# Optimization experiments

Hardware: AMD Instinct MI355X
Metric: run time of the kernel (lower is better)

The kernel has to match this reference:

```python
import jax, jax.numpy as jnp
import numpy as np

N, K, DN, DA, H = 20000, 16, 128, 128, 256
D_IN = DN + DA  # 256


def _lin_init(key, out_dim, in_dim):
    scale = 1.0 / np.sqrt(in_dim)
    return jax.random.uniform(key, (out_dim, in_dim), jnp.float32, -scale, scale)


def setup_inputs() -> dict:
    key = jax.random.key(0)
    ks = jax.random.split(key, 16)
    # adjacency: col 0 = parent index; cols 1..K = neighbor indices, -1 padded.
    parent = jax.random.randint(ks[0], (N, 1), 0, N, dtype=jnp.int32)
    nbr_first = jax.random.randint(ks[1], (N, 1), 0, N, dtype=jnp.int32)  # guarantee >=1 nbr
    nbr_rest = jax.random.randint(ks[2], (N, K - 1), -1, N, dtype=jnp.int32)
    adj = jnp.concatenate([parent, nbr_first, nbr_rest], axis=1)
    names = jax.random.normal(ks[3], (N, DN), jnp.float32)
    attrs = jax.random.normal(ks[4], (N, DA), jnp.float32)
    return {
        "nodeAdjacencySpecTensor": adj,
        "nodeNamesEncoded": names,
        "nodeAttributesEncoded": attrs,
        "W_in": _lin_init(ks[5], H, D_IN),
        "b_in": jnp.zeros((H,), jnp.float32),
        "W_parent": _lin_init(ks[6], H, H),
        "b_parent": jnp.zeros((H,), jnp.float32),
        "W_neighbor": _lin_init(ks[7], H, H),
        "b_neighbor": jnp.zeros((H,), jnp.float32),
        "W_ih": _lin_init(ks[8], 3 * H, H),
        "b_ih": jnp.zeros((3 * H,), jnp.float32),
        "W_hh": _lin_init(ks[9], 3 * H, H),
        "b_hh": jnp.zeros((3 * H,), jnp.float32),
        "depth": 3,
    }


def _gru_cell(x, h, W_ih, b_ih, W_hh, b_hh):
    # torch.nn.GRUCell math; gate order r, z, n.
    gi = x @ W_ih.T + b_ih
    gh = h @ W_hh.T + b_hh
    i_r, i_z, i_n = jnp.split(gi, 3, axis=-1)
    h_r, h_z, h_n = jnp.split(gh, 3, axis=-1)
    r = jax.nn.sigmoid(i_r + h_r)
    z = jax.nn.sigmoid(i_z + h_z)
    n = jnp.tanh(i_n + r * h_n)
    return (1.0 - z) * n + z * h


def reference(nodeAdjacencySpecTensor, nodeNamesEncoded, nodeAttributesEncoded,
              W_in, b_in, W_parent, b_parent, W_neighbor, b_neighbor,
              W_ih, b_ih, W_hh, b_hh, depth):
    adj = nodeAdjacencySpecTensor
    parent_idx = adj[:, 0]                 # [N]
    nbr_idx = adj[:, 1:]                   # [N, K], -1 padded
    mask = (nbr_idx >= 0)                  # [N, K]
    safe_nbr = jnp.clip(nbr_idx, 0, None)
    nbr_count = jnp.maximum(mask.sum(axis=1), 1).astype(jnp.float32)  # [N]

    node_info = jnp.concatenate([nodeNamesEncoded, nodeAttributesEncoded], axis=-1)
    x = node_info @ W_in.T + b_in          # [N, H]

    for _ in range(depth):
        p = x @ W_parent.T + b_parent      # [N, H]
        nbr = x @ W_neighbor.T + b_neighbor  # [N, H]
        # irregular gathers
        parent_feat = p[parent_idx]        # [N, H]
        gathered = nbr[safe_nbr]           # [N, K, H]
        nbr_sum = jnp.sum(gathered * mask[:, :, None], axis=1)  # [N, H]
        summary = parent_feat + nbr_sum / nbr_count[:, None]
        x = _gru_cell(x, summary, W_ih, b_ih, W_hh, b_hh)
    return x
```

## Files before the change

kernel.cpp:

```cpp
#include <hip/hip_runtime.h>
#include <hip/hip_bf16.h>

typedef __bf16 bf16x8 __attribute__((ext_vector_type(8)));
typedef __bf16 bf16x4 __attribute__((ext_vector_type(4)));
typedef float  f32x4  __attribute__((ext_vector_type(4)));

#define NN   20000
#define NADJ 17

__device__ __forceinline__ void xcd_remap(int b, int nwg, int col_shift, int& r, int& c)
{
    int q = nwg >> 3, rem = nwg & 7;
    int x = b & 7, k = b >> 3;
    int start = x * q + (x < rem ? x : rem);
    int idx = start + k;
    r = idx >> col_shift;
    c = idx & ((1 << col_shift) - 1);
}

__global__ void pack_weights_kernel(const float* __restrict__ Win, const float* __restrict__ bin,
                                    const float* __restrict__ Wp,  const float* __restrict__ bp,
                                    const float* __restrict__ Wn,  const float* __restrict__ bn,
                                    const float* __restrict__ Wih, const float* __restrict__ bih,
                                    const float* __restrict__ Whh, const float* __restrict__ bhh,
                                    __bf16* __restrict__ Wb, float* __restrict__ bc)
{
    int idx = blockIdx.x * 256 + threadIdx.x;
    if (idx < 1536) {
        int c = idx; float v;
        if (c < 256)      v = bin[c];
        else if (c < 512) { int j = c - 256; v = bp[j] + bn[j]; }
        else {
            int rel = c - 512;
            int j = (rel >> 6) * 16 + (rel & 15);
            int g = (rel >> 4) & 3;
            if      (g == 0) v = bih[j] + bhh[j];
            else if (g == 1) v = bih[256 + j] + bhh[256 + j];
            else if (g == 2) v = bih[512 + j];
            else             v = bhh[512 + j];
        }
        bc[c] = v;
    }
    if (idx >= 180224) return;
    int e = idx << 2;
    const float* src = nullptr;
    bool zero = false;
    if (e < 65536) {
        int row = e >> 8, k = e & 255;
        src = Win + (size_t)row * 256 + k;
    } else if (e < 196608) {
        int rel = e - 65536;
        int row = rel >> 9, k = rel & 511;
        src = (k < 256) ? (Wp + (size_t)row * 256 + k)
                        : (Wn + (size_t)row * 256 + (k - 256));
    } else {
        int rel = e - 196608;
        int row = rel >> 9, k = rel & 511;
        int j = (row >> 6) * 16 + (row & 15);
        int g = (row >> 4) & 3;
        if (k < 256) {
            if (g == 3) zero = true;
            else {
                int off = (g == 0) ? 0 : (g == 1) ? 256 : 512;
                src = Wih + (size_t)(off + j) * 256 + k;
            }
        } else {
            int k2 = k - 256;
            if (g == 2) zero = true;
            else {
                int off = (g == 0) ? 0 : (g == 1) ? 256 : 512;
                src = Whh + (size_t)(off + j) * 256 + k2;
            }
        }
    }
    float4 v = zero ? make_float4(0.f, 0.f, 0.f, 0.f) : *(const float4*)src;
    bf16x4 o = { (__bf16)v.x, (__bf16)v.y, (__bf16)v.z, (__bf16)v.w };
    *(bf16x4*)(Wb + (size_t)e) = o;
}

__global__ void pack_info_kernel(const float* __restrict__ names, const float* __restrict__ attrs,
                                 __bf16* __restrict__ xb)
{
    int idx = blockIdx.x * 256 + threadIdx.x;
    if (idx >= NN * 64) return;
    int i  = idx >> 6;
    int d4 = (idx & 63) << 2;
    const float* src = (d4 < 128) ? (names + (size_t)i * 128 + d4)
                                  : (attrs + (size_t)i * 128 + (d4 - 128));
    float4 v = *(const float4*)src;
    bf16x4 o = { (__bf16)v.x, (__bf16)v.y, (__bf16)v.z, (__bf16)v.w };
    *(bf16x4*)(xb + (size_t)i * 256 + d4) = o;
}

__global__ void gather_avg_kernel(const int* __restrict__ adj, const __bf16* __restrict__ x,
                                  __bf16* __restrict__ G2)
{
    const int node = blockIdx.x * 4 + (threadIdx.x >> 6);
    const int l = threadIdx.x & 63;
    int av = (l < NADJ) ? adj[(size_t)node * NADJ + l] : -1;
    float s0 = 0.f, s1 = 0.f, s2 = 0.f, s3 = 0.f;
    int cnt = 0;
#pragma unroll
    for (int j = 1; j < NADJ; ++j) {
        int idx = __shfl(av, j, 64);
        if (idx >= 0) {
            ++cnt;
            bf16x4 v = *(const bf16x4*)(x + (size_t)idx * 256 + l * 4);
            s0 += (float)v[0]; s1 += (float)v[1]; s2 += (float)v[2]; s3 += (float)v[3];
        }
    }
    float inv = 1.f / (float)(cnt < 1 ? 1 : cnt);
    bf16x4 o = { (__bf16)(s0 * inv), (__bf16)(s1 * inv), (__bf16)(s2 * inv), (__bf16)(s3 * inv) };
    *(bf16x4*)(G2 + (size_t)node * 256 + l * 4) = o;
}

__global__ __launch_bounds__(256, 4)
void gemm_bias_kernel(const __bf16* __restrict__ A0, const __bf16* __restrict__ A1, int lda,
                      const int* __restrict__ parents, int par_stride,
                      const __bf16* __restrict__ W, int ldw,
                      const float* __restrict__ bias,
                      float* __restrict__ C, __bf16* __restrict__ Cb,
                      int n_rows, int n_cols, int kt_n, int nwg, int col_shift)
{
    __shared__ __align__(16) __bf16 As[128 * 64];
    __shared__ __align__(16) __bf16 Bs[128 * 64];
    __shared__ int par_s[128];
    const int t = threadIdx.x;
    const int w = t >> 6;
    const int l = t & 63;
    int rb, cb_;
    xcd_remap(blockIdx.x, nwg, col_shift, rb, cb_);
    const int brow = rb * 128;
    const int bcol = cb_ * 128;
    const int wr = (w >> 1) * 64, wc = (w & 1) * 64;

    if (parents) {
        if (t < 128) {
            int node = brow + t; if (node > n_rows - 1) node = n_rows - 1;
            par_s[t] = parents[(size_t)node * par_stride];
        }
        __syncthreads();
    }

    f32x4 acc[4][4] = {};

    for (int kt = 0; kt < kt_n; ++kt) {
        const int k0 = kt * 64;
#pragma unroll
        for (int i = 0; i < 4; ++i) {
            int f   = i * 256 + t;
            int row = f >> 3;
            int cs  = ((f & 7) * 16) ^ ((row & 7) << 4);
            int ar  = brow + row; if (ar > n_rows - 1) ar = n_rows - 1;
            const __bf16* abase;
            if (parents && k0 < 256)             abase = A0 + (size_t)par_s[row] * 256 + k0;
            else if (A1 != nullptr && k0 >= 256) abase = A1 + (size_t)ar * 256 + (k0 - 256);
            else                                 abase = A0 + (size_t)ar * lda + k0;
            const __bf16* ga = abase + (cs >> 1);
            const __bf16* gb = W + (size_t)(bcol + row) * ldw + k0 + (cs >> 1);
            char* la = (char*)As + (i * 256 + w * 64) * 16;
            char* lb = (char*)Bs + (i * 256 + w * 64) * 16;
            __builtin_amdgcn_global_load_lds(
                (const __attribute__((address_space(1))) unsigned int*)ga,
                (__attribute__((address_space(3))) unsigned int*)la, 16, 0, 0);
            __builtin_amdgcn_global_load_lds(
                (const __attribute__((address_space(1))) unsigned int*)gb,
                (__attribute__((address_space(3))) unsigned int*)lb, 16, 0, 0);
        }
        asm volatile("s_waitcnt vmcnt(0)" ::: "memory");
        __syncthreads();
#pragma unroll
        for (int ks = 0; ks < 2; ++ks) {
            bf16x8 af[4], bfv[4];
#pragma unroll
            for (int m = 0; m < 4; ++m) {
                int row = wr + m * 16 + (l & 15);
                int cb  = (ks * 64 + ((l >> 4) * 16)) ^ ((row & 7) << 4);
                af[m] = *(const bf16x8*)((const char*)As + row * 128 + cb);
            }
#pragma unroll
            for (int n = 0; n < 4; ++n) {
                int row = wc + n * 16 + (l & 15);
                int cb  = (ks * 64 + ((l >> 4) * 16)) ^ ((row & 7) << 4);
                bfv[n] = *(const bf16x8*)((const char*)Bs + row * 128 + cb);
            }
#pragma unroll
            for (int m = 0; m < 4; ++m)
#pragma unroll
                for (int n = 0; n < 4; ++n)
                    acc[m][n] = __builtin_amdgcn_mfma_f32_16x16x32_bf16(af[m], bfv[n], acc[m][n], 0, 0, 0);
        }
        __syncthreads();
    }
#pragma unroll
    for (int m = 0; m < 4; ++m) {
        int r0 = brow + wr + m * 16 + ((l >> 4) * 4);
#pragma unroll
        for (int n = 0; n < 4; ++n) {
            int c = bcol + wc + n * 16 + (l & 15);
            float bv = bias[c];
#pragma unroll
            for (int i = 0; i < 4; ++i) {
                int r = r0 + i;
                if (r < n_rows) {
                    float v = acc[m][n][i] + bv;
                    if (C)  C[(size_t)r * n_cols + c]  = v;
                    if (Cb) Cb[(size_t)r * n_cols + c] = (__bf16)v;
                }
            }
        }
    }
}

#define GRU_KT_BODY(K0, ABASE, SKIP_N)                                                  \
    {                                                                                   \
        _Pragma("unroll")                                                               \
        for (int i = 0; i < 4; ++i) {                                                   \
            int f   = i * 256 + t;                                                      \
            int row = f >> 3;                                                           \
            int cs  = ((f & 7) * 16) ^ ((row & 7) << 4);                                \
            int ar  = brow + row; if (ar > n_rows - 1) ar = n_rows - 1;                 \
            const __bf16* ga = (ABASE) + (size_t)ar * 256 + (cs >> 1);                  \
            const __bf16* gb = W + (size_t)(bcol + row) * 512 + (K0) + (cs >> 1);       \
            char* la = (char*)As + (i * 256 + w * 64) * 16;                             \
            char* lb = (char*)Bs + (i * 256 + w * 64) * 16;                             \
            __builtin_amdgcn_global_load_lds(                                           \
                (const __attribute__((address_space(1))) unsigned int*)ga,              \
                (__attribute__((address_space(3))) unsigned int*)la, 16, 0, 0);         \
            if (((row >> 4) & 3) != (SKIP_N))                                           \
                __builtin_amdgcn_global_load_lds(                                       \
                    (const __attribute__((address_space(1))) unsigned int*)gb,          \
                    (__attribute__((address_space(3))) unsigned int*)lb, 16, 0, 0);     \
        }                                                                               \
        asm volatile("s_waitcnt vmcnt(0)" ::: "memory");                                \
        __syncthreads();                                                                \
        _Pragma("unroll")                                                               \
        for (int ks = 0; ks < 2; ++ks) {                                                \
            bf16x8 af[4], bfv[4];                                                       \
            _Pragma("unroll")                                                           \
            for (int m = 0; m < 4; ++m) {                                               \
                int row = wr + m * 16 + (l & 15);                                       \
                int cb  = (ks * 64 + ((l >> 4) * 16)) ^ ((row & 7) << 4);               \
                af[m] = *(const bf16x8*)((const char*)As + row * 128 + cb);             \
            }                                                                           \
            _Pragma("unroll")                                                           \
            for (int n = 0; n < 4; ++n) {                                               \
                if (n == (SKIP_N)) continue;                                            \
                int row = wc + n * 16 + (l & 15);                                       \
                int cb  = (ks * 64 + ((l >> 4) * 16)) ^ ((row & 7) << 4);               \
                bfv[n] = *(const bf16x8*)((const char*)Bs + row * 128 + cb);            \
            }                                                                           \
            _Pragma("unroll")                                                           \
            for (int m = 0; m < 4; ++m)                                                 \
                _Pragma("unroll")                                                       \
                for (int n = 0; n < 4; ++n)                                             \
                    if (n != (SKIP_N))                                                  \
                        acc[m][n] = __builtin_amdgcn_mfma_f32_16x16x32_bf16(            \
                            af[m], bfv[n], acc[m][n], 0, 0, 0);                         \
        }                                                                               \
        __syncthreads();                                                                \
    }

__global__ __launch_bounds__(256, 4)
void gru_gemm_kernel(const __bf16* __restrict__ A0, const __bf16* __restrict__ A1,
                     const __bf16* __restrict__ W,
                     const float* __restrict__ bias,
                     const float* __restrict__ SUM,
                     float* __restrict__ X, __bf16* __restrict__ xb_next,
                     int n_rows)
{
    __shared__ __align__(16) __bf16 As[128 * 64];
    __shared__ __align__(16) __bf16 Bs[128 * 64];
    const int t = threadIdx.x;
    const int w = t >> 6;
    const int l = t & 63;
    int rb, cb_;
    xcd_remap(blockIdx.x, 157 * 8, 3, rb, cb_);
    const int brow = rb * 128;
    const int bcol = cb_ * 128;
    const int wr = (w >> 1) * 64, wc = (w & 1) * 64;

    f32x4 acc[4][4] = {};

    for (int kt = 0; kt < 4; ++kt) {
        const int k0 = kt * 64;
        GRU_KT_BODY(k0, A0 + k0, 3)
    }
    for (int kt = 4; kt < 8; ++kt) {
        const int k0 = kt * 64;
        GRU_KT_BODY(k0, A1 + (k0 - 256), 2)
    }

    const int jb = ((bcol + wc) >> 6) * 16 + (l & 15);
    const int c0 = bcol + wc + (l & 15);
    const float b0 = bias[c0], b1 = bias[c0 + 16], b2 = bias[c0 + 32], b3 = bias[c0 + 48];
#pragma unroll
    for (int m = 0; m < 4; ++m) {
        int r0 = brow + wr + m * 16 + ((l >> 4) * 4);
#pragma unroll
        for (int i = 0; i < 4; ++i) {
            int r = r0 + i;
            if (r < n_rows) {
                float gr  = acc[m][0][i] + b0;
                float gz  = acc[m][1][i] + b1;
                float gin = acc[m][2][i] + b2;
                float ghn = acc[m][3][i] + b3;
                float rg = 1.f / (1.f + __expf(-gr));
                float zg = 1.f / (1.f + __expf(-gz));
                float a2 = gin + rg * ghn;
                float tt = __expf(-2.f * fabsf(a2));
                float ng = (1.f - tt) / (1.f + tt);
                ng = (a2 < 0.f) ? -ng : ng;
                float h = SUM[(size_t)r * 256 + jb];
                float out = (1.f - zg) * ng + zg * h;
                if (X)       X[(size_t)r * 256 + jb] = out;
                if (xb_next) xb_next[(size_t)r * 256 + jb] = (__bf16)out;
            }
        }
    }
}

extern "C" void kernel_launch(void* const* d_in, const int* in_sizes, int n_in,
                              void* d_out, int out_size, void* d_ws, size_t ws_size,
                              hipStream_t stream)
{
    const int*   adj   = (const int*)  d_in[0];
    const float* names = (const float*)d_in[1];
    const float* attrs = (const float*)d_in[2];
    const float* Win = (const float*)d_in[3];
    const float* bin = (const float*)d_in[4];
    const float* Wp  = (const float*)d_in[5];
    const float* bp  = (const float*)d_in[6];
    const float* Wn  = (const float*)d_in[7];
    const float* bn  = (const float*)d_in[8];
    const float* Wih = (const float*)d_in[9];
    const float* bih = (const float*)d_in[10];
    const float* Whh = (const float*)d_in[11];
    const float* bhh = (const float*)d_in[12];
    float* X = (float*)d_out;

    char* w = (char*)d_ws;
    __bf16* xinfo = (__bf16*)(w);
    __bf16* xb0   = (__bf16*)(w + 10240000);
    __bf16* xb1   = (__bf16*)(w + 20480000);
    __bf16* sb    = (__bf16*)(w + 30720000);
    __bf16* G2    = (__bf16*)(w + 40960000);
    float*  SUM   = (float*) (w + 51200000);
    __bf16* Wb    = (__bf16*)(w + 71680000);
    float*  bc    = (float*) (w + 73121792);

    pack_weights_kernel<<<704, 256, 0, stream>>>(Win, bin, Wp, bp, Wn, bn, Wih, bih, Whh, bhh, Wb, bc);
    pack_info_kernel<<<5000, 256, 0, stream>>>(names, attrs, xinfo);

    gemm_bias_kernel<<<314, 256, 0, stream>>>(xinfo, nullptr, 256, nullptr, 0,
                                              Wb, 256, bc, nullptr, xb0, NN, 256, 4, 314, 1);

    __bf16* cur = xb0;
    __bf16* nxt = xb1;
    for (int d = 0; d < 3; ++d) {
        gather_avg_kernel<<<5000, 256, 0, stream>>>(adj, cur, G2);
        gemm_bias_kernel<<<314, 256, 0, stream>>>(cur, G2, 256, adj, NADJ,
                                                  Wb + 65536, 512, bc + 256,
                                                  SUM, sb, NN, 256, 8, 314, 1);
        gru_gemm_kernel<<<1256, 256, 0, stream>>>(cur, sb, Wb + 196608, bc + 512,
                                                  SUM, (d == 2) ? X : nullptr,
                                                  (d < 2) ? nxt : nullptr, NN);
        __bf16* tmp = cur; cur = nxt; nxt = tmp;
    }
}
```

Baseline: 265.4 us.

## Fuse neighbor gather-average into summary GEMM and split summary into bf16 hi/lo

Each summary-GEMM block now gathers and averages its 64 rows' neighbor features straight into LDS, then runs the parent/neighbor GEMM with a full 256-column weight tile. This removes the separate gather kernel and the G2 round trip through global memory. The fp32 SUM buffer is replaced by a bf16 hi/lo pair, which cuts write traffic while keeping near-fp32 precision for the GRU hidden term. In exchange, the fused kernel runs only 313 blocks of 512 threads with large LDS use, so occupancy and latency hiding may be limited.

Result: slower. 314.0 us (+18.3%).

```diff
diff --git a/kernel.cpp b/kernel.cpp
--- a/kernel.cpp
+++ b/kernel.cpp
@@ -92,39 +92,15 @@
     *(bf16x4*)(xb + (size_t)i * 256 + d4) = o;
 }
 
-__global__ void gather_avg_kernel(const int* __restrict__ adj, const __bf16* __restrict__ x,
-                                  __bf16* __restrict__ G2)
-{
-    const int node = blockIdx.x * 4 + (threadIdx.x >> 6);
-    const int l = threadIdx.x & 63;
-    int av = (l < NADJ) ? adj[(size_t)node * NADJ + l] : -1;
-    float s0 = 0.f, s1 = 0.f, s2 = 0.f, s3 = 0.f;
-    int cnt = 0;
-#pragma unroll
-    for (int j = 1; j < NADJ; ++j) {
-        int idx = __shfl(av, j, 64);
-        if (idx >= 0) {
-            ++cnt;
-            bf16x4 v = *(const bf16x4*)(x + (size_t)idx * 256 + l * 4);
-            s0 += (float)v[0]; s1 += (float)v[1]; s2 += (float)v[2]; s3 += (float)v[3];
-        }
-    }
-    float inv = 1.f / (float)(cnt < 1 ? 1 : cnt);
-    bf16x4 o = { (__bf16)(s0 * inv), (__bf16)(s1 * inv), (__bf16)(s2 * inv), (__bf16)(s3 * inv) };
-    *(bf16x4*)(G2 + (size_t)node * 256 + l * 4) = o;
-}
-
 __global__ __launch_bounds__(256, 4)
-void gemm_bias_kernel(const __bf16* __restrict__ A0, const __bf16* __restrict__ A1, int lda,
-                      const int* __restrict__ parents, int par_stride,
+void gemm_bias_kernel(const __bf16* __restrict__ A0, int lda,
                       const __bf16* __restrict__ W, int ldw,
                       const float* __restrict__ bias,
-                      float* __restrict__ C, __bf16* __restrict__ Cb,
+                      __bf16* __restrict__ Cb,
                       int n_rows, int n_cols, int kt_n, int nwg, int col_shift)
 {
     __shared__ __align__(16) __bf16 As[128 * 64];
     __shared__ __align__(16) __bf16 Bs[128 * 64];
-    __shared__ int par_s[128];
     const int t = threadIdx.x;
     const int w = t >> 6;
     const int l = t & 63;
@@ -134,14 +110,6 @@
     const int bcol = cb_ * 128;
     const int wr = (w >> 1) * 64, wc = (w & 1) * 64;
 
-    if (parents) {
-        if (t < 128) {
-            int node = brow + t; if (node > n_rows - 1) node = n_rows - 1;
-            par_s[t] = parents[(size_t)node * par_stride];
-        }
-        __syncthreads();
-    }
-
     f32x4 acc[4][4] = {};
 
     for (int kt = 0; kt < kt_n; ++kt) {
@@ -152,11 +120,7 @@
             int row = f >> 3;
             int cs  = ((f & 7) * 16) ^ ((row & 7) << 4);
             int ar  = brow + row; if (ar > n_rows - 1) ar = n_rows - 1;
-            const __bf16* abase;
-            if (parents && k0 < 256)             abase = A0 + (size_t)par_s[row] * 256 + k0;
-            else if (A1 != nullptr && k0 >= 256) abase = A1 + (size_t)ar * 256 + (k0 - 256);
-            else                                 abase = A0 + (size_t)ar * lda + k0;
-            const __bf16* ga = abase + (cs >> 1);
+            const __bf16* ga = A0 + (size_t)ar * lda + k0 + (cs >> 1);
             const __bf16* gb = W + (size_t)(bcol + row) * ldw + k0 + (cs >> 1);
             char* la = (char*)As + (i * 256 + w * 64) * 16;
             char* lb = (char*)Bs + (i * 256 + w * 64) * 16;
@@ -202,10 +166,118 @@
 #pragma unroll
             for (int i = 0; i < 4; ++i) {
                 int r = r0 + i;
+                if (r < n_rows) Cb[(size_t)r * n_cols + c] = (__bf16)(acc[m][n][i] + bv);
+            }
+        }
+    }
+}
+
+__global__ __launch_bounds__(512, 4)
+void summary_fused_kernel(const int* __restrict__ adj, const __bf16* __restrict__ x,
+                          const __bf16* __restrict__ Wps, const float* __restrict__ bias,
+                          __bf16* __restrict__ sbh, __bf16* __restrict__ sbl, int n_rows)
+{
+    __shared__ __align__(16) __bf16 Gs[4 * 64 * 64];
+    __shared__ __align__(16) __bf16 As[64 * 64];
+    __shared__ __align__(16) __bf16 Bs[256 * 64];
+    __shared__ int par_s[64];
+    const int t = threadIdx.x;
+    const int w = t >> 6;
+    const int l = t & 63;
+    const int brow = blockIdx.x * 64;
+
+#pragma unroll
+    for (int q = 0; q < 8; ++q) {
+        int rr = w * 8 + q;
+        int node = brow + rr; if (node > n_rows - 1) node = n_rows - 1;
+        int av = (l < NADJ) ? adj[(size_t)node * NADJ + l] : -1;
+        if (l == 0) par_s[rr] = av;
+        float s0 = 0.f, s1 = 0.f, s2 = 0.f, s3 = 0.f;
+        int cnt = 0;
+#pragma unroll
+        for (int j = 1; j < NADJ; ++j) {
+            int idx = __shfl(av, j, 64);
+            if (idx >= 0) {
+                ++cnt;
+                bf16x4 v = *(const bf16x4*)(x + (size_t)idx * 256 + l * 4);
+                s0 += (float)v[0]; s1 += (float)v[1]; s2 += (float)v[2]; s3 += (float)v[3];
+            }
+        }
+        float inv = 1.f / (float)(cnt < 1 ? 1 : cnt);
+        bf16x4 o = { (__bf16)(s0 * inv), (__bf16)(s1 * inv), (__bf16)(s2 * inv), (__bf16)(s3 * inv) };
+        *(bf16x4*)((char*)Gs + (l >> 4) * 8192 + rr * 128 + ((((l & 15) * 8)) ^ ((rr & 7) << 4))) = o;
+    }
+    __syncthreads();
+
+    const int wr = (w >> 2) * 32, wc = (w & 3) * 64;
+    f32x4 acc[2][4] = {};
+
+    for (int kt = 0; kt < 8; ++kt) {
+        const int k0 = kt * 64;
+        if (kt < 4) {
+            int row = t >> 3;
+            int cs  = ((t & 7) * 16) ^ ((row & 7) << 4);
+            const __bf16* ga = x + (size_t)par_s[row] * 256 + k0 + (cs >> 1);
+            char* la = (char*)As + (w * 64) * 16;
+            __builtin_amdgcn_global_load_lds(
+                (const __attribute__((address_space(1))) unsigned int*)ga,
+                (__attribute__((address_space(3))) unsigned int*)la, 16, 0, 0);
+        }
+#pragma unroll
+        for (int i = 0; i < 4; ++i) {
+            int f   = i * 512 + t;
+            int row = f >> 3;
+            int cs  = ((f & 7) * 16) ^ ((row & 7) << 4);
+            const __bf16* gb = Wps + (size_t)row * 512 + k0 + (cs >> 1);
+            char* lb = (char*)Bs + (i * 512 + w * 64) * 16;
+            __builtin_amdgcn_global_load_lds(
+                (const __attribute__((address_space(1))) unsigned int*)gb,
+                (__attribute__((address_space(3))) unsigned int*)lb, 16, 0, 0);
+        }
+        asm volatile("s_waitcnt vmcnt(0)" ::: "memory");
+        __syncthreads();
+#pragma unroll
+        for (int ks = 0; ks < 2; ++ks) {
+            bf16x8 af[2], bfv[4];
+#pragma unroll
+            for (int m = 0; m < 2; ++m) {
+                int row = wr + m * 16 + (l & 15);
+                int cb  = (ks * 64 + ((l >> 4) * 16)) ^ ((row & 7) << 4);
+                const char* base = (kt < 4) ? ((const char*)As + row * 128)
+                                            : ((const char*)Gs + (kt - 4) * 8192 + row * 128);
+                af[m] = *(const bf16x8*)(base + cb);
+            }
+#pragma unroll
+            for (int n = 0; n < 4; ++n) {
+                int row = wc + n * 16 + (l & 15);
+                int cb  = (ks * 64 + ((l >> 4) * 16)) ^ ((row & 7) << 4);
+                bfv[n] = *(const bf16x8*)((const char*)Bs + row * 128 + cb);
+            }
+#pragma unroll
+            for (int m = 0; m < 2; ++m)
+#pragma unroll
+                for (int n = 0; n < 4; ++n)
+                    acc[m][n] = __builtin_amdgcn_mfma_f32_16x16x32_bf16(af[m], bfv[n], acc[m][n], 0, 0, 0);
+        }
+        __syncthreads();
+    }
+
+#pragma unroll
+    for (int m = 0; m < 2; ++m) {
+        int r0 = brow + wr + m * 16 + ((l >> 4) * 4);
+#pragma unroll
+        for (int n = 0; n < 4; ++n) {
+            int c = wc + n * 16 + (l & 15);
+            float bv = bias[c];
+#pragma unroll
+            for (int i = 0; i < 4; ++i) {
+                int r = r0 + i;
                 if (r < n_rows) {
                     float v = acc[m][n][i] + bv;
-                    if (C)  C[(size_t)r * n_cols + c]  = v;
-                    if (Cb) Cb[(size_t)r * n_cols + c] = (__bf16)v;
+                    __bf16 hi = (__bf16)v;
+                    float lo = v - (float)hi;
+                    sbh[(size_t)r * 256 + c] = hi;
+                    sbl[(size_t)r * 256 + c] = (__bf16)lo;
                 }
             }
         }
@@ -265,7 +337,7 @@
 void gru_gemm_kernel(const __bf16* __restrict__ A0, const __bf16* __restrict__ A1,
                      const __bf16* __restrict__ W,
                      const float* __restrict__ bias,
-                     const float* __restrict__ SUM,
+                     const __bf16* __restrict__ sbh, const __bf16* __restrict__ sbl,
                      float* __restrict__ X, __bf16* __restrict__ xb_next,
                      int n_rows)
 {
@@ -311,7 +383,7 @@
                 float tt = __expf(-2.f * fabsf(a2));
                 float ng = (1.f - tt) / (1.f + tt);
                 ng = (a2 < 0.f) ? -ng : ng;
-                float h = SUM[(size_t)r * 256 + jb];
+                float h = (float)sbh[(size_t)r * 256 + jb] + (float)sbl[(size_t)r * 256 + jb];
                 float out = (1.f - zg) * ng + zg * h;
                 if (X)       X[(size_t)r * 256 + jb] = out;
                 if (xb_next) xb_next[(size_t)r * 256 + jb] = (__bf16)out;
@@ -343,27 +415,23 @@
     __bf16* xinfo = (__bf16*)(w);
     __bf16* xb0   = (__bf16*)(w + 10240000);
     __bf16* xb1   = (__bf16*)(w + 20480000);
-    __bf16* sb    = (__bf16*)(w + 30720000);
-    __bf16* G2    = (__bf16*)(w + 40960000);
-    float*  SUM   = (float*) (w + 51200000);
-    __bf16* Wb    = (__bf16*)(w + 71680000);
-    float*  bc    = (float*) (w + 73121792);
+    __bf16* sbh   = (__bf16*)(w + 30720000);
+    __bf16* sbl   = (__bf16*)(w + 40960000);
+    __bf16* Wb    = (__bf16*)(w + 51200000);
+    float*  bc    = (float*) (w + 52641792);
 
     pack_weights_kernel<<<704, 256, 0, stream>>>(Win, bin, Wp, bp, Wn, bn, Wih, bih, Whh, bhh, Wb, bc);
     pack_info_kernel<<<5000, 256, 0, stream>>>(names, attrs, xinfo);
 
-    gemm_bias_kernel<<<314, 256, 0, stream>>>(xinfo, nullptr, 256, nullptr, 0,
-                                              Wb, 256, bc, nullptr, xb0, NN, 256, 4, 314, 1);
+    gemm_bias_kernel<<<314, 256, 0, stream>>>(xinfo, 256, Wb, 256, bc, xb0, NN, 256, 4, 314, 1);
 
     __bf16* cur = xb0;
     __bf16* nxt = xb1;
     for (int d = 0; d < 3; ++d) {
-        gather_avg_kernel<<<5000, 256, 0, stream>>>(adj, cur, G2);
-        gemm_bias_kernel<<<314, 256, 0, stream>>>(cur, G2, 256, adj, NADJ,
-                                                  Wb + 65536, 512, bc + 256,
-                                                  SUM, sb, NN, 256, 8, 314, 1);
-        gru_gemm_kernel<<<1256, 256, 0, stream>>>(cur, sb, Wb + 196608, bc + 512,
-                                                  SUM, (d == 2) ? X : nullptr,
+        summary_fused_kernel<<<313, 512, 0, stream>>>(adj, cur, Wb + 65536, bc + 256,
+                                                      sbh, sbl, NN);
+        gru_gemm_kernel<<<1256, 256, 0, stream>>>(cur, sbh, Wb + 196608, bc + 512,
+                                                  sbh, sbl, (d == 2) ? X : nullptr,
                                                   (d < 2) ? nxt : nullptr, NN);
         __bf16* tmp = cur; cur = nxt; nxt = tmp;
     }
```
